# Performance work log

Measured on AMD Instinct MI355X. Metric: run time of the kernel, lower is better.

Reference implementation:

```python
import jax, jax.numpy as jnp
import numpy as np

DIM = 384
HEADS = 8
EPS = 1e-5


def _layernorm(x, g, b):
    mu = jnp.mean(x, axis=-1, keepdims=True)
    var = jnp.mean(jnp.square(x - mu), axis=-1, keepdims=True)
    return (x - mu) * jax.lax.rsqrt(var + EPS) * g + b


def setup_inputs() -> dict:
    key = jax.random.key(0)
    ks = jax.random.split(key, 16)
    d = DIM
    s = lambda k, shape, scale=0.02: jax.random.normal(k, shape, dtype=jnp.float32) * scale
    return {
        "x": jax.random.normal(ks[0], (16, d, 32, 32), dtype=jnp.float32),
        "pos_w": s(ks[1], (d, 1, 3, 3), 0.1),   # depthwise conv kernel (OIHW, I=1)
        "pos_b": jnp.zeros((d,), jnp.float32),
        "g1": jnp.ones((d,), jnp.float32),
        "b1": jnp.zeros((d,), jnp.float32),
        "wqkv": s(ks[2], (d, 3 * d)),
        "bqkv": jnp.zeros((3 * d,), jnp.float32),
        "wproj": s(ks[3], (d, d)),
        "bproj": jnp.zeros((d,), jnp.float32),
        "g2": jnp.ones((d,), jnp.float32),
        "b2": jnp.zeros((d,), jnp.float32),
        "w1": s(ks[4], (d, 4 * d)),
        "bf1": jnp.zeros((4 * d,), jnp.float32),
        "w2": s(ks[5], (4 * d, d)),
        "bf2": jnp.zeros((d,), jnp.float32),
    }


def reference(x, pos_w, pos_b, g1, b1, wqkv, bqkv, wproj, bproj, g2, b2, w1, bf1, w2, bf2):
    B, C, H, W = x.shape
    # depthwise 3x3 conv positional embedding, residual
    pe = jax.lax.conv_general_dilated(
        x, pos_w, window_strides=(1, 1), padding=((1, 1), (1, 1)),
        dimension_numbers=("NCHW", "OIHW", "NCHW"), feature_group_count=C)
    x = x + pe + pos_b[None, :, None, None]
    # to tokens [B, N, C]
    t = x.reshape(B, C, H * W).transpose(0, 2, 1)
    N = H * W
    Dh = C // HEADS
    # attention
    xn = _layernorm(t, g1, b1)
    qkv = xn @ wqkv + bqkv                                   # [B,N,3C]
    qkv = qkv.reshape(B, N, 3, HEADS, Dh)
    q, k, v = qkv[:, :, 0], qkv[:, :, 1], qkv[:, :, 2]        # [B,N,H,Dh]
    scale = Dh ** -0.5
    attn = jnp.einsum("bqhd,bkhd->bhqk", q, k) * scale
    attn = jax.nn.softmax(attn, axis=-1)
    o = jnp.einsum("bhqk,bkhd->bqhd", attn, v).reshape(B, N, C)
    t = t + o @ wproj + bproj
    # MLP
    yn = _layernorm(t, g2, b2)
    h = jax.nn.gelu(yn @ w1 + bf1, approximate=False)
    t = t + h @ w2 + bf2
    return t.transpose(0, 2, 1).reshape(B, C, H, W)
```

## Files before the change

### kernel.cpp

```cpp
#include <hip/hip_runtime.h>
#include <hip/hip_bf16.h>
#include <math.h>

#define BATCH 16
#define CDIM 384
#define HH 32
#define WW 32
#define NPIX 1024
#define MTOK (BATCH * NPIX)
#define NHEADS 8
#define DH 48
#define QKVN (3 * CDIM)
#define FFN (4 * CDIM)

typedef unsigned short u16;
typedef unsigned int u32;
typedef __attribute__((ext_vector_type(8))) short short8;
typedef __attribute__((ext_vector_type(4))) float floatx4;

#define MFMA16(a, b, c) __builtin_amdgcn_mfma_f32_16x16x32_bf16(a, b, c, 0, 0, 0)

__device__ __forceinline__ void gl2lds16(const void* g, void* l) {
    __builtin_amdgcn_global_load_lds(
        (const __attribute__((address_space(1))) void*)g,
        (__attribute__((address_space(3))) void*)l, 16, 0, 0);
}

__global__ __launch_bounds__(256) void conv_pe_kernel(const float* __restrict__ x,
                                                      const float* __restrict__ pos_w,
                                                      const float* __restrict__ pos_b,
                                                      float* __restrict__ t) {
    __shared__ float xs[64][100];
    __shared__ float os[32][68];
    const int cg = blockIdx.x, h = blockIdx.y, b = blockIdx.z;
    const int tid = threadIdx.x;
    const int c0 = cg * 64;

#pragma unroll
    for (int it = 0; it < 6; ++it) {
        int task = tid + it * 256;
        int c = task / 24, rem = task % 24;
        int row = rem >> 3, f4 = rem & 7;
        int hh = h + row - 1;
        float4 v = {0.f, 0.f, 0.f, 0.f};
        if (hh >= 0 && hh < HH)
            v = *(const float4*)(x + (((size_t)(b * CDIM + c0 + c) * HH + hh) * WW + f4 * 4));
        *(float4*)&xs[c][row * 32 + f4 * 4] = v;
    }
    __syncthreads();

    const int c = tid >> 2, w0 = (tid & 3) * 8;
    float wgt[9];
#pragma unroll
    for (int i = 0; i < 9; ++i) wgt[i] = pos_w[(c0 + c) * 9 + i];
    const float pb = pos_b[c0 + c];
#pragma unroll
    for (int wi = 0; wi < 8; ++wi) {
        int w = w0 + wi;
        float acc = 0.f;
#pragma unroll
        for (int r = 0; r < 3; ++r)
#pragma unroll
            for (int kw = 0; kw < 3; ++kw) {
                int w2 = w + kw - 1;
                if (w2 >= 0 && w2 < WW) acc += xs[c][r * 32 + w2] * wgt[r * 3 + kw];
            }
        os[w][c] = xs[c][32 + w] + acc + pb;
    }
    __syncthreads();

    float* dstb = t + (size_t)(b * NPIX + h * 32) * CDIM + c0;
#pragma unroll
    for (int it = 0; it < 2; ++it) {
        int task = tid + it * 256;
        int px = task >> 4, f4 = task & 15;
        *(float4*)(dstb + (size_t)px * CDIM + f4 * 4) = *(const float4*)&os[px][f4 * 4];
    }
}

__global__ void ln_kernel(const float* __restrict__ in,
                          const float* __restrict__ g,
                          const float* __restrict__ bta,
                          __hip_bfloat16* __restrict__ out) {
    int m = blockIdx.x;
    const float* row = in + (size_t)m * CDIM;
    int tid = threadIdx.x;
    float v0 = row[tid], v1 = row[tid + 128], v2 = row[tid + 256];
    float s = v0 + v1 + v2;
    float ss = v0 * v0 + v1 * v1 + v2 * v2;
#pragma unroll
    for (int off = 32; off > 0; off >>= 1) {
        s += __shfl_down(s, off, 64);
        ss += __shfl_down(ss, off, 64);
    }
    __shared__ float red[4];
    if ((tid & 63) == 0) { red[tid >> 6] = s; red[2 + (tid >> 6)] = ss; }
    __syncthreads();
    float sum = red[0] + red[1], sumsq = red[2] + red[3];
    float mu = sum * (1.f / CDIM);
    float var = sumsq * (1.f / CDIM) - mu * mu;
    float rstd = rsqrtf(var + 1e-5f);
    __hip_bfloat16* orow = out + (size_t)m * CDIM;
    orow[tid]       = __float2bfloat16((v0 - mu) * rstd * g[tid] + bta[tid]);
    orow[tid + 128] = __float2bfloat16((v1 - mu) * rstd * g[tid + 128] + bta[tid + 128]);
    orow[tid + 256] = __float2bfloat16((v2 - mu) * rstd * g[tid + 256] + bta[tid + 256]);
}

__global__ void wt_kernel(const float* __restrict__ W, __hip_bfloat16* __restrict__ Wt,
                          int K, int N) {
    __shared__ float tile[32][33];
    int n0 = blockIdx.x * 32, k0 = blockIdx.y * 32;
    int tx = threadIdx.x & 31, ty = threadIdx.x >> 5;
    for (int i = ty; i < 32; i += 8) tile[i][tx] = W[(size_t)(k0 + i) * N + n0 + tx];
    __syncthreads();
    for (int i = ty; i < 32; i += 8)
        Wt[(size_t)(n0 + i) * K + k0 + tx] = __float2bfloat16(tile[tx][i]);
}

__global__ __launch_bounds__(256) void vtrans_kernel(const u16* __restrict__ qkv,
                                                     u16* __restrict__ vT) {
    __shared__ u16 Vl[48][136];
    const int kt = blockIdx.x, h = blockIdx.y, b = blockIdx.z;
    const int tid = threadIdx.x;
    const size_t base = (size_t)b * NPIX * QKVN + 2 * CDIM + (size_t)h * DH;
#pragma unroll
    for (int it = 0; it < 3; ++it) {
        int task = tid + it * 256;
        int key = task / 6, ch = task - key * 6;
        short8 v = *(const short8*)(qkv + base + (size_t)(kt * 128 + key) * QKVN + ch * 8);
#pragma unroll
        for (int i = 0; i < 8; ++i) Vl[ch * 8 + i][key] = (u16)v[i];
    }
    __syncthreads();
    u16* dst = vT + (size_t)(b * NHEADS + h) * DH * NPIX + (size_t)kt * 128;
#pragma unroll
    for (int it = 0; it < 3; ++it) {
        int task = tid + it * 256;
        int d = task >> 4, ch = task & 15;
        short8 v = *(const short8*)&Vl[d][ch * 8];
        *(short8*)(dst + (size_t)d * NPIX + ch * 8) = v;
    }
}

template <int RES, int ACT, int OUTBF>
__global__ __launch_bounds__(256) void gemm_bf16(
    const u16* __restrict__ A, const u16* __restrict__ Bt,
    const float* __restrict__ bias, const float* __restrict__ Res,
    void* __restrict__ Cout, int N, int K) {
    __shared__ u16 As[2][2][128 * 32];
    __shared__ u16 Bs[2][2][64 * 32];
    const int tid = threadIdx.x;
    const int lane = tid & 63;
    const int wv = tid >> 6;
    const int qd = lane >> 4;
    const int l16 = lane & 15;
    const int wy = wv >> 1, wx = wv & 1;

    const int id = blockIdx.x;
    const int xcd = id & 7, j = id >> 3;
    const int m0 = (xcd * 16 + (j & 15)) * 128;
    const int n0 = (j >> 4) * 64;

    const int rr = tid >> 2, cc = (tid & 3) * 8;
    const u16* Ag = A + (size_t)(m0 + rr) * K + cc;
    const u16* Bg = Bt + (size_t)(n0 + rr) * K + cc;

    const floatx4 fz = {0.f, 0.f, 0.f, 0.f};
    floatx4 acc[4][2];
#pragma unroll
    for (int i = 0; i < 4; ++i)
#pragma unroll
        for (int jj = 0; jj < 2; ++jj) acc[i][jj] = fz;

    auto stage = [&](int slot, int k0) {
#pragma unroll
        for (int kc = 0; kc < 2; ++kc) {
            gl2lds16(Ag + k0 + kc * 32, &As[slot][kc][0] + tid * 8);
            gl2lds16(Ag + (size_t)64 * K + k0 + kc * 32, &As[slot][kc][0] + 2048 + tid * 8);
            gl2lds16(Bg + k0 + kc * 32, &Bs[slot][kc][0] + tid * 8);
        }
    };

    stage(0, 0);
    const int iters = K >> 6;
    for (int it = 0; it < iters; ++it) {
        const int slot = it & 1;
        __syncthreads();
        if (it + 1 < iters) stage(slot ^ 1, (it + 1) << 6);
#pragma unroll
        for (int kc = 0; kc < 2; ++kc) {
            short8 af[4], bfr[2];
#pragma unroll
            for (int i = 0; i < 4; ++i)
                af[i] = *(const short8*)(&As[slot][kc][0] + (wy * 64 + i * 16 + l16) * 32 + qd * 8);
#pragma unroll
            for (int jj = 0; jj < 2; ++jj)
                bfr[jj] = *(const short8*)(&Bs[slot][kc][0] + (wx * 32 + jj * 16 + l16) * 32 + qd * 8);
#pragma unroll
            for (int i = 0; i < 4; ++i)
#pragma unroll
                for (int jj = 0; jj < 2; ++jj) acc[i][jj] = MFMA16(af[i], bfr[jj], acc[i][jj]);
        }
    }

    const int colb = n0 + wx * 32 + l16;
    const int rowb = m0 + wy * 64 + qd * 4;
#pragma unroll
    for (int jj = 0; jj < 2; ++jj) {
        int col = colb + jj * 16;
        float bb = bias[col];
#pragma unroll
        for (int i = 0; i < 4; ++i) {
            int row = rowb + i * 16;
#pragma unroll
            for (int r = 0; r < 4; ++r) {
                float c = acc[i][jj][r] + bb;
                if (RES) c += Res[(size_t)(row + r) * N + col];
                if (ACT) c = 0.5f * c * (1.f + erff(c * 0.70710678118654752f));
                if (OUTBF)
                    ((__hip_bfloat16*)Cout)[(size_t)(row + r) * N + col] = __float2bfloat16(c);
                else
                    ((float*)Cout)[(size_t)(row + r) * N + col] = c;
            }
        }
    }
}

__global__ __launch_bounds__(256) void attn_kernel(const u16* __restrict__ qkv,
                                                   const u16* __restrict__ vT,
                                                   __hip_bfloat16* __restrict__ ob) {
    const int id = blockIdx.x;
    const int h = id & 7;
    const int b = (id >> 3) & 15;
    const int qb = id >> 7;
    const int tid = threadIdx.x;
    const int lane = tid & 63, wv = tid >> 6;
    const int qd = lane >> 4, l16 = lane & 15;

    __shared__ u16 Kl[65][48];
    __shared__ u16 Vt[48][72];
    __shared__ __hip_bfloat16 Pl[4][32][72];

    if (tid < 24) ((u32*)&Kl[64][0])[tid] = 0;

    const size_t bh = (size_t)b * NPIX * QKVN + (size_t)h * DH;
    const u16* vtb = vT + (size_t)(b * NHEADS + h) * DH * NPIX;

    short8 qf[2][2];
    const short8 z8 = {0, 0, 0, 0, 0, 0, 0, 0};
#pragma unroll
    for (int g = 0; g < 2; ++g) {
        const u16* gq = qkv + bh + (size_t)(qb * 128 + wv * 32 + g * 16 + l16) * QKVN;
        qf[g][0] = *(const short8*)(gq + qd * 8);
        qf[g][1] = (qd < 2) ? *(const short8*)(gq + 32 + qd * 8) : z8;
    }

    const floatx4 fz = {0.f, 0.f, 0.f, 0.f};
    floatx4 o[2][3];
    float lsum[2][4];
#pragma unroll
    for (int g = 0; g < 2; ++g) {
#pragma unroll
        for (int nt = 0; nt < 3; ++nt) o[g][nt] = fz;
#pragma unroll
        for (int r = 0; r < 4; ++r) lsum[g][r] = 0.f;
    }
    const float scale = 0.14433756729740643f;

    for (int kt = 0; kt < 16; ++kt) {
        __syncthreads();
        {
            const size_t kbase = bh + (size_t)(kt * 64) * QKVN + CDIM;
            int key = tid / 6, ch = tid - key * 6;
            gl2lds16(qkv + kbase + (size_t)key * QKVN + ch * 8, &Kl[0][0] + tid * 8);
            if (tid < 128) {
                int t2 = tid + 256;
                int k2 = t2 / 6, c2 = t2 - k2 * 6;
                gl2lds16(qkv + kbase + (size_t)k2 * QKVN + c2 * 8, &Kl[0][0] + t2 * 8);
            }
            int d = tid >> 3, vc = tid & 7;
            short8 v0 = *(const short8*)(vtb + (size_t)d * NPIX + kt * 64 + vc * 8);
            *(short8*)&Vt[d][vc * 8] = v0;
            if (tid < 128) {
                int d1 = (tid + 256) >> 3;
                short8 v1 = *(const short8*)(vtb + (size_t)d1 * NPIX + kt * 64 + vc * 8);
                *(short8*)&Vt[d1][vc * 8] = v1;
            }
        }
        __syncthreads();

        short8 kl[4], kh[4];
#pragma unroll
        for (int t = 0; t < 4; ++t) {
            const u16* kr = &Kl[0][0] + (t * 16 + l16) * 48;
            kl[t] = *(const short8*)(kr + qd * 8);
            kh[t] = *(const short8*)(kr + 32 + qd * 8);
        }
        floatx4 s[2][4];
#pragma unroll
        for (int g = 0; g < 2; ++g)
#pragma unroll
            for (int t = 0; t < 4; ++t) {
                floatx4 a = fz;
                a = MFMA16(qf[g][0], kl[t], a);
                a = MFMA16(qf[g][1], kh[t], a);
                s[g][t] = a;
            }

#pragma unroll
        for (int g = 0; g < 2; ++g)
#pragma unroll
            for (int t = 0; t < 4; ++t) {
#pragma unroll
                for (int r = 0; r < 4; ++r) {
                    float p = __expf(s[g][t][r] * scale);
                    Pl[wv][g * 16 + qd * 4 + r][t * 16 + l16] = __float2bfloat16(p);
                    lsum[g][r] += p;
                }
            }

        short8 vl[3], vh[3];
#pragma unroll
        for (int nt = 0; nt < 3; ++nt) {
            const u16* vr = &Vt[0][0] + (nt * 16 + l16) * 72;
            vl[nt] = *(const short8*)(vr + qd * 8);
            vh[nt] = *(const short8*)(vr + 32 + qd * 8);
        }
#pragma unroll
        for (int g = 0; g < 2; ++g) {
            const __hip_bfloat16* prr = &Pl[wv][g * 16 + l16][0];
            short8 ap0 = *(const short8*)(prr + qd * 8);
            short8 ap1 = *(const short8*)(prr + 32 + qd * 8);
#pragma unroll
            for (int nt = 0; nt < 3; ++nt) {
                o[g][nt] = MFMA16(ap0, vl[nt], o[g][nt]);
                o[g][nt] = MFMA16(ap1, vh[nt], o[g][nt]);
            }
        }
    }

#pragma unroll
    for (int g = 0; g < 2; ++g)
#pragma unroll
        for (int r = 0; r < 4; ++r) {
            float l = lsum[g][r];
            l += __shfl_xor(l, 1, 64);
            l += __shfl_xor(l, 2, 64);
            l += __shfl_xor(l, 4, 64);
            l += __shfl_xor(l, 8, 64);
            float inv = 1.f / l;
            size_t row = (size_t)(b * NPIX + qb * 128 + wv * 32 + g * 16 + qd * 4 + r) * CDIM + h * DH;
#pragma unroll
            for (int nt = 0; nt < 3; ++nt)
                ob[row + nt * 16 + l16] = __float2bfloat16(o[g][nt][r] * inv);
        }
}

__global__ void transpose_kernel(const float* __restrict__ t, float* __restrict__ out) {
    __shared__ float tile[32][33];
    int b = blockIdx.z;
    int n0 = blockIdx.x * 32;
    int c0 = blockIdx.y * 32;
    int tx = threadIdx.x & 31;
    int ty = threadIdx.x >> 5;
    for (int i = ty; i < 32; i += 8)
        tile[i][tx] = t[(size_t)(b * NPIX + n0 + i) * CDIM + c0 + tx];
    __syncthreads();
    int c = threadIdx.x >> 3, f4 = threadIdx.x & 7;
    float4 v;
    v.x = tile[f4 * 4 + 0][c];
    v.y = tile[f4 * 4 + 1][c];
    v.z = tile[f4 * 4 + 2][c];
    v.w = tile[f4 * 4 + 3][c];
    *(float4*)(out + (size_t)(b * CDIM + c0 + c) * NPIX + n0 + f4 * 4) = v;
}

extern "C" void kernel_launch(void* const* d_in, const int* in_sizes, int n_in,
                              void* d_out, int out_size, void* d_ws, size_t ws_size,
                              hipStream_t stream) {
    const float* x = (const float*)d_in[0];
    const float* pos_w = (const float*)d_in[1];
    const float* pos_b = (const float*)d_in[2];
    const float* g1 = (const float*)d_in[3];
    const float* b1 = (const float*)d_in[4];
    const float* wqkv = (const float*)d_in[5];
    const float* bqkv = (const float*)d_in[6];
    const float* wproj = (const float*)d_in[7];
    const float* bproj = (const float*)d_in[8];
    const float* g2 = (const float*)d_in[9];
    const float* b2 = (const float*)d_in[10];
    const float* w1 = (const float*)d_in[11];
    const float* bf1 = (const float*)d_in[12];
    const float* w2 = (const float*)d_in[13];
    const float* bf2 = (const float*)d_in[14];
    float* out = (float*)d_out;

    char* ws = (char*)d_ws;
    float* t = (float*)ws;
    __hip_bfloat16* xn = (__hip_bfloat16*)(ws + 25165824);
    u16* vTb = (u16*)xn;
    __hip_bfloat16* wqkvT = (__hip_bfloat16*)(ws + 37748736);
    __hip_bfloat16* wprojT = (__hip_bfloat16*)(ws + 38633472);
    __hip_bfloat16* w1T = (__hip_bfloat16*)(ws + 38928384);
    __hip_bfloat16* w2T = (__hip_bfloat16*)(ws + 40108032);
    char* big = ws + 41287680;
    u16* qkvb = (u16*)big;
    __hip_bfloat16* obb = (__hip_bfloat16*)(big + 37748736);
    u16* hb = (u16*)big;

    wt_kernel<<<dim3(QKVN / 32, CDIM / 32), 256, 0, stream>>>(wqkv, wqkvT, CDIM, QKVN);
    wt_kernel<<<dim3(CDIM / 32, CDIM / 32), 256, 0, stream>>>(wproj, wprojT, CDIM, CDIM);
    wt_kernel<<<dim3(FFN / 32, CDIM / 32), 256, 0, stream>>>(w1, w1T, CDIM, FFN);
    wt_kernel<<<dim3(CDIM / 32, FFN / 32), 256, 0, stream>>>(w2, w2T, FFN, CDIM);

    conv_pe_kernel<<<dim3(CDIM / 64, HH, BATCH), 256, 0, stream>>>(x, pos_w, pos_b, t);
    ln_kernel<<<MTOK, 128, 0, stream>>>(t, g1, b1, xn);
    gemm_bf16<0, 0, 1><<<dim3(128 * (QKVN / 64)), 256, 0, stream>>>(
        (const u16*)xn, (const u16*)wqkvT, bqkv, nullptr, qkvb, QKVN, CDIM);
    vtrans_kernel<<<dim3(NPIX / 128, NHEADS, BATCH), 256, 0, stream>>>(qkvb, vTb);
    attn_kernel<<<dim3(1024), 256, 0, stream>>>(qkvb, vTb, obb);
    gemm_bf16<1, 0, 0><<<dim3(128 * (CDIM / 64)), 256, 0, stream>>>(
        (const u16*)obb, (const u16*)wprojT, bproj, t, t, CDIM, CDIM);
    ln_kernel<<<MTOK, 128, 0, stream>>>(t, g2, b2, xn);
    gemm_bf16<0, 1, 1><<<dim3(128 * (FFN / 64)), 256, 0, stream>>>(
        (const u16*)xn, (const u16*)w1T, bf1, nullptr, hb, FFN, CDIM);
    gemm_bf16<1, 0, 0><<<dim3(128 * (CDIM / 64)), 256, 0, stream>>>(
        (const u16*)hb, (const u16*)w2T, bf2, t, t, CDIM, FFN);
    transpose_kernel<<<dim3(32, 12, BATCH), 256, 0, stream>>>(t, out);
}
```

Measured before the change: 346.5 us.

## Template GEMM tile sizes and double-buffer K/V loads in attention

The GEMM kernel is templated on the N-tile and K-step sizes. The QKV and FC1 GEMMs now use 128x128 tiles with a K-step of 32, which doubles per-block reuse of A and halves the grid. The attention kernel double-buffers K in LDS and prefetches the next V tile into registers, so global loads for tile kt+1 overlap the compute on tile kt. This costs more LDS and register pressure, and the larger GEMM tiles leave fewer blocks to fill the GPU.

```diff
diff --git a/kernel.cpp b/kernel.cpp
--- a/kernel.cpp
+++ b/kernel.cpp
@@ -142,13 +142,15 @@
     }
 }
 
-template <int RES, int ACT, int OUTBF>
+template <int BN, int BK, int RES, int ACT, int OUTBF>
 __global__ __launch_bounds__(256) void gemm_bf16(
     const u16* __restrict__ A, const u16* __restrict__ Bt,
     const float* __restrict__ bias, const float* __restrict__ Res,
     void* __restrict__ Cout, int N, int K) {
-    __shared__ u16 As[2][2][128 * 32];
-    __shared__ u16 Bs[2][2][64 * 32];
+    constexpr int KC = BK / 32;
+    constexpr int NF = BN / 32;
+    __shared__ u16 As[2][KC][128 * 32];
+    __shared__ u16 Bs[2][KC][BN * 32];
     const int tid = threadIdx.x;
     const int lane = tid & 63;
     const int wv = tid >> 6;
@@ -159,54 +161,55 @@
     const int id = blockIdx.x;
     const int xcd = id & 7, j = id >> 3;
     const int m0 = (xcd * 16 + (j & 15)) * 128;
-    const int n0 = (j >> 4) * 64;
+    const int n0 = (j >> 4) * BN;
 
     const int rr = tid >> 2, cc = (tid & 3) * 8;
     const u16* Ag = A + (size_t)(m0 + rr) * K + cc;
     const u16* Bg = Bt + (size_t)(n0 + rr) * K + cc;
 
     const floatx4 fz = {0.f, 0.f, 0.f, 0.f};
-    floatx4 acc[4][2];
+    floatx4 acc[4][NF];
 #pragma unroll
     for (int i = 0; i < 4; ++i)
 #pragma unroll
-        for (int jj = 0; jj < 2; ++jj) acc[i][jj] = fz;
+        for (int jj = 0; jj < NF; ++jj) acc[i][jj] = fz;
 
     auto stage = [&](int slot, int k0) {
 #pragma unroll
-        for (int kc = 0; kc < 2; ++kc) {
+        for (int kc = 0; kc < KC; ++kc) {
             gl2lds16(Ag + k0 + kc * 32, &As[slot][kc][0] + tid * 8);
             gl2lds16(Ag + (size_t)64 * K + k0 + kc * 32, &As[slot][kc][0] + 2048 + tid * 8);
             gl2lds16(Bg + k0 + kc * 32, &Bs[slot][kc][0] + tid * 8);
+            if (NF == 4) gl2lds16(Bg + (size_t)64 * K + k0 + kc * 32, &Bs[slot][kc][0] + 2048 + tid * 8);
         }
     };
 
     stage(0, 0);
-    const int iters = K >> 6;
+    const int iters = K / BK;
     for (int it = 0; it < iters; ++it) {
         const int slot = it & 1;
         __syncthreads();
-        if (it + 1 < iters) stage(slot ^ 1, (it + 1) << 6);
-#pragma unroll
-        for (int kc = 0; kc < 2; ++kc) {
-            short8 af[4], bfr[2];
+        if (it + 1 < iters) stage(slot ^ 1, (it + 1) * BK);
+#pragma unroll
+        for (int kc = 0; kc < KC; ++kc) {
+            short8 af[4], bfr[NF];
 #pragma unroll
             for (int i = 0; i < 4; ++i)
                 af[i] = *(const short8*)(&As[slot][kc][0] + (wy * 64 + i * 16 + l16) * 32 + qd * 8);
 #pragma unroll
-            for (int jj = 0; jj < 2; ++jj)
-                bfr[jj] = *(const short8*)(&Bs[slot][kc][0] + (wx * 32 + jj * 16 + l16) * 32 + qd * 8);
+            for (int jj = 0; jj < NF; ++jj)
+                bfr[jj] = *(const short8*)(&Bs[slot][kc][0] + (wx * (BN / 2) + jj * 16 + l16) * 32 + qd * 8);
 #pragma unroll
             for (int i = 0; i < 4; ++i)
 #pragma unroll
-                for (int jj = 0; jj < 2; ++jj) acc[i][jj] = MFMA16(af[i], bfr[jj], acc[i][jj]);
-        }
-    }
-
-    const int colb = n0 + wx * 32 + l16;
+                for (int jj = 0; jj < NF; ++jj) acc[i][jj] = MFMA16(af[i], bfr[jj], acc[i][jj]);
+        }
+    }
+
+    const int colb = n0 + wx * (BN / 2) + l16;
     const int rowb = m0 + wy * 64 + qd * 4;
 #pragma unroll
-    for (int jj = 0; jj < 2; ++jj) {
+    for (int jj = 0; jj < NF; ++jj) {
         int col = colb + jj * 16;
         float bb = bias[col];
 #pragma unroll
@@ -237,14 +240,31 @@
     const int lane = tid & 63, wv = tid >> 6;
     const int qd = lane >> 4, l16 = lane & 15;
 
-    __shared__ u16 Kl[65][48];
+    __shared__ u16 Kl[2][65][48];
     __shared__ u16 Vt[48][72];
     __shared__ __hip_bfloat16 Pl[4][32][72];
 
-    if (tid < 24) ((u32*)&Kl[64][0])[tid] = 0;
+    if (tid < 24) { ((u32*)&Kl[0][64][0])[tid] = 0; ((u32*)&Kl[1][64][0])[tid] = 0; }
 
     const size_t bh = (size_t)b * NPIX * QKVN + (size_t)h * DH;
     const u16* vtb = vT + (size_t)(b * NHEADS + h) * DH * NPIX;
+
+    auto stageK = [&](int kt, int slot) {
+        const size_t kbase = bh + (size_t)(kt * 64) * QKVN + CDIM;
+        int key = tid / 6, ch = tid - key * 6;
+        gl2lds16(qkv + kbase + (size_t)key * QKVN + ch * 8, &Kl[slot][0][0] + tid * 8);
+        if (tid < 128) {
+            int t2 = tid + 256;
+            int k2 = t2 / 6, c2 = t2 - k2 * 6;
+            gl2lds16(qkv + kbase + (size_t)k2 * QKVN + c2 * 8, &Kl[slot][0][0] + t2 * 8);
+        }
+    };
+    const int vd = tid >> 3, vc = tid & 7, vd1 = (tid + 256) >> 3;
+    short8 vA, vB;
+    auto loadV = [&](int kt) {
+        vA = *(const short8*)(vtb + (size_t)vd * NPIX + kt * 64 + vc * 8);
+        if (tid < 128) vB = *(const short8*)(vtb + (size_t)vd1 * NPIX + kt * 64 + vc * 8);
+    };
 
     short8 qf[2][2];
     const short8 z8 = {0, 0, 0, 0, 0, 0, 0, 0};
@@ -267,32 +287,21 @@
     }
     const float scale = 0.14433756729740643f;
 
+    stageK(0, 0);
+    loadV(0);
+
     for (int kt = 0; kt < 16; ++kt) {
+        const int cur = kt & 1;
         __syncthreads();
-        {
-            const size_t kbase = bh + (size_t)(kt * 64) * QKVN + CDIM;
-            int key = tid / 6, ch = tid - key * 6;
-            gl2lds16(qkv + kbase + (size_t)key * QKVN + ch * 8, &Kl[0][0] + tid * 8);
-            if (tid < 128) {
-                int t2 = tid + 256;
-                int k2 = t2 / 6, c2 = t2 - k2 * 6;
-                gl2lds16(qkv + kbase + (size_t)k2 * QKVN + c2 * 8, &Kl[0][0] + t2 * 8);
-            }
-            int d = tid >> 3, vc = tid & 7;
-            short8 v0 = *(const short8*)(vtb + (size_t)d * NPIX + kt * 64 + vc * 8);
-            *(short8*)&Vt[d][vc * 8] = v0;
-            if (tid < 128) {
-                int d1 = (tid + 256) >> 3;
-                short8 v1 = *(const short8*)(vtb + (size_t)d1 * NPIX + kt * 64 + vc * 8);
-                *(short8*)&Vt[d1][vc * 8] = v1;
-            }
-        }
+        *(short8*)&Vt[vd][vc * 8] = vA;
+        if (tid < 128) *(short8*)&Vt[vd1][vc * 8] = vB;
         __syncthreads();
+        if (kt + 1 < 16) { stageK(kt + 1, cur ^ 1); loadV(kt + 1); }
 
         short8 kl[4], kh[4];
 #pragma unroll
         for (int t = 0; t < 4; ++t) {
-            const u16* kr = &Kl[0][0] + (t * 16 + l16) * 48;
+            const u16* kr = &Kl[cur][0][0] + (t * 16 + l16) * 48;
             kl[t] = *(const short8*)(kr + qd * 8);
             kh[t] = *(const short8*)(kr + 32 + qd * 8);
         }
@@ -415,16 +424,16 @@
 
     conv_pe_kernel<<<dim3(CDIM / 64, HH, BATCH), 256, 0, stream>>>(x, pos_w, pos_b, t);
     ln_kernel<<<MTOK, 128, 0, stream>>>(t, g1, b1, xn);
-    gemm_bf16<0, 0, 1><<<dim3(128 * (QKVN / 64)), 256, 0, stream>>>(
+    gemm_bf16<128, 32, 0, 0, 1><<<dim3(128 * (QKVN / 128)), 256, 0, stream>>>(
         (const u16*)xn, (const u16*)wqkvT, bqkv, nullptr, qkvb, QKVN, CDIM);
     vtrans_kernel<<<dim3(NPIX / 128, NHEADS, BATCH), 256, 0, stream>>>(qkvb, vTb);
     attn_kernel<<<dim3(1024), 256, 0, stream>>>(qkvb, vTb, obb);
-    gemm_bf16<1, 0, 0><<<dim3(128 * (CDIM / 64)), 256, 0, stream>>>(
+    gemm_bf16<64, 64, 1, 0, 0><<<dim3(128 * (CDIM / 64)), 256, 0, stream>>>(
         (const u16*)obb, (const u16*)wprojT, bproj, t, t, CDIM, CDIM);
     ln_kernel<<<MTOK, 128, 0, stream>>>(t, g2, b2, xn);
-    gemm_bf16<0, 1, 1><<<dim3(128 * (FFN / 64)), 256, 0, stream>>>(
+    gemm_bf16<128, 32, 0, 1, 1><<<dim3(128 * (FFN / 128)), 256, 0, stream>>>(
         (const u16*)xn, (const u16*)w1T, bf1, nullptr, hb, FFN, CDIM);
-    gemm_bf16<1, 0, 0><<<dim3(128 * (CDIM / 64)), 256, 0, stream>>>(
+    gemm_bf16<64, 64, 1, 0, 0><<<dim3(128 * (CDIM / 64)), 256, 0, stream>>>(
         (const u16*)hb, (const u16*)w2T, bf2, t, t, CDIM, FFN);
     transpose_kernel<<<dim3(32, 12, BATCH), 256, 0, stream>>>(t, out);
 }
```

Measured after the change: 341.2 us. About the same (-1.5%).
